# Optimization experiments

Measured on AMD Instinct MI355X. Metric: run time of the kernel, lower is better.

The kernel has to match this reference:

```python
import jax, jax.numpy as jnp
import numpy as np

D_IN = 1024
D_OUT = 1024
B = 4
S = 2048


def setup_inputs() -> dict:
    key = jax.random.key(0)
    kx, kq, kk, kv = jax.random.split(key, 4)
    x = jax.random.normal(kx, (B, S, D_IN), dtype=jnp.float32)
    # Linear weights stored as [d_in, d_out] so projection is x @ W
    sc = 1.0 / np.sqrt(D_IN)
    Wq = jax.random.normal(kq, (D_IN, D_OUT), dtype=jnp.float32) * sc
    Wk = jax.random.normal(kk, (D_IN, D_OUT), dtype=jnp.float32) * sc
    Wv = jax.random.normal(kv, (D_IN, D_OUT), dtype=jnp.float32) * sc
    return {"x": x, "Wq": Wq, "Wk": Wk, "Wv": Wv}


def reference(x, Wq, Wk, Wv):
    # q, k, v: [b, s, d_out]
    q = jnp.einsum("bsd,de->bse", x, Wq)
    k = jnp.einsum("bsd,de->bse", x, Wk)
    v = jnp.einsum("bsd,de->bse", x, Wv)
    s = q.shape[1]
    # raw scores [b, s, s]
    scores = jnp.einsum("bqd,bkd->bqk", q, k)
    # causal mask: disallow key j > query i (see notes re: original mask bug)
    causal = jnp.triu(jnp.ones((s, s), dtype=bool), k=1)
    scores = jnp.where(causal[None, :, :], -jnp.inf, scores)
    scale = 1.0 / jnp.sqrt(jnp.asarray(k.shape[-1], dtype=scores.dtype))
    att_weights = jax.nn.softmax(scores * scale, axis=-1)
    # dropout p=0.0 -> identity
    att_output = jnp.einsum("bqk,bkd->bqd", att_weights, v)
    return att_output, att_weights
```

## Files before the change

### kernel.cpp

```cpp
#include <hip/hip_runtime.h>
#include <stdint.h>

#define DIM 1024
#define SEQ 2048
#define NB 4

typedef unsigned short u16;
typedef __bf16 bf16x8 __attribute__((ext_vector_type(8)));
typedef float floatx4 __attribute__((ext_vector_type(4)));

__device__ __forceinline__ u16 f32_to_bf16(float f) {
  union { float f; unsigned u; } v; v.f = f;
  unsigned r = v.u + 0x7FFFu + ((v.u >> 16) & 1u);
  return (u16)(r >> 16);
}

__device__ __forceinline__ void async16(const void* g, void* l) {
  __builtin_amdgcn_global_load_lds(
      (__attribute__((address_space(1))) unsigned int*)g,
      (__attribute__((address_space(3))) unsigned int*)l, 16, 0, 0);
}

__global__ __launch_bounds__(256) void k_prep(const float* __restrict__ x,
                                              const float* __restrict__ Wq,
                                              const float* __restrict__ Wk,
                                              const float* __restrict__ Wv,
                                              u16* __restrict__ xb,
                                              u16* __restrict__ wt) {
  __shared__ u16 tile[32][33];
  const int bid = blockIdx.x;
  const int tid = threadIdx.x;
  if (bid < 4096) {
    int i = bid * 256 + tid;
    float4 a = ((const float4*)x)[i * 2];
    float4 b = ((const float4*)x)[i * 2 + 1];
    ushort4 o0, o1;
    o0.x = f32_to_bf16(a.x); o0.y = f32_to_bf16(a.y);
    o0.z = f32_to_bf16(a.z); o0.w = f32_to_bf16(a.w);
    o1.x = f32_to_bf16(b.x); o1.y = f32_to_bf16(b.y);
    o1.z = f32_to_bf16(b.z); o1.w = f32_to_bf16(b.w);
    ((ushort4*)xb)[i * 2] = o0;
    ((ushort4*)xb)[i * 2 + 1] = o1;
  } else {
    int t = bid - 4096;
    int z = t >> 10;
    int ti = t & 1023;
    int c0 = (ti & 31) * 32, r0 = (ti >> 5) * 32;
    const float* src = (z == 0) ? Wq : (z == 1) ? Wk : Wv;
    u16* d = wt + (size_t)z * DIM * DIM;
    int tx = tid & 31, ty = tid >> 5;
    #pragma unroll
    for (int dy = 0; dy < 32; dy += 8)
      tile[ty + dy][tx] = f32_to_bf16(src[(size_t)(r0 + ty + dy) * DIM + c0 + tx]);
    __syncthreads();
    #pragma unroll
    for (int dy = 0; dy < 32; dy += 8)
      d[(size_t)(c0 + ty + dy) * DIM + r0 + tx] = tile[tx][ty + dy];
  }
}

__device__ __forceinline__ void mfma_core(const u16* __restrict__ A, int lda,
                                          const u16* __restrict__ Bt, int ldb,
                                          int ktiles, u16* lds,
                                          floatx4 acc[4][4]) {
  const int tid = threadIdx.x;
  const int lane = tid & 63;
  const int wid = tid >> 6;
  u16* lds_a = lds;
  u16* lds_b = lds + 8192;

  const int srow = lane >> 3;
  const int sg = (lane & 7) ^ (srow & 7);
  const u16* ag = A + (size_t)(wid * 32 + srow) * lda + sg * 8;
  const u16* bg = Bt + (size_t)(wid * 32 + srow) * ldb + sg * 8;
  u16* la = lds_a + wid * 2048;
  u16* lb = lds_b + wid * 2048;

  const int wm = (wid >> 1) * 64, wn = (wid & 1) * 64;
  const int lrow = lane & 15, quad = lane >> 4;
  const int s = lrow & 7;
  const int g0 = (quad ^ s) * 8;
  const int g1 = ((quad + 4) ^ s) * 8;
  const u16* pa = lds_a + (wm + lrow) * 64;
  const u16* pb = lds_b + (wn + lrow) * 64;

  for (int kt = 0; kt < ktiles; ++kt) {
    #pragma unroll
    for (int c = 0; c < 4; ++c) {
      async16(ag + (size_t)c * 8 * lda, la + c * 512);
      async16(bg + (size_t)c * 8 * ldb, lb + c * 512);
    }
    ag += 64; bg += 64;
    __syncthreads();
    #pragma unroll
    for (int ks = 0; ks < 2; ++ks) {
      const int g = ks ? g1 : g0;
      bf16x8 af[4], bfr[4];
      #pragma unroll
      for (int t = 0; t < 4; ++t) af[t] = *(const bf16x8*)(pa + t * 1024 + g);
      #pragma unroll
      for (int t = 0; t < 4; ++t) bfr[t] = *(const bf16x8*)(pb + t * 1024 + g);
      #pragma unroll
      for (int i = 0; i < 4; ++i)
        #pragma unroll
        for (int j = 0; j < 4; ++j)
          acc[i][j] = __builtin_amdgcn_mfma_f32_16x16x32_bf16(af[i], bfr[j],
                                                              acc[i][j], 0, 0, 0);
    }
    __syncthreads();
  }
}

__device__ __forceinline__ void mfma_core128(const u16* __restrict__ A, int lda,
                                             const u16* __restrict__ Bt, int ldb,
                                             int kchunks, u16* lds,
                                             floatx4 acc[4][4]) {
  const int tid = threadIdx.x;
  const int lane = tid & 63;
  const int wid = tid >> 6;
  u16* lds_a = lds;
  u16* lds_b = lds + 16384;

  const int srow4 = lane >> 4;
  const int sgr = lane & 15;
  const int gbase = sgr ^ srow4;
  const u16* ag0 = A + (size_t)(wid * 32 + srow4) * lda + gbase * 8;
  const u16* ag1 = A + (size_t)(wid * 32 + srow4) * lda + (gbase ^ 4) * 8;
  const u16* bg0 = Bt + (size_t)(wid * 32 + srow4) * ldb + gbase * 8;
  const u16* bg1 = Bt + (size_t)(wid * 32 + srow4) * ldb + (gbase ^ 4) * 8;
  u16* la = lds_a + wid * 4096;
  u16* lb = lds_b + wid * 4096;

  const int wm = (wid >> 1) * 64, wn = (wid & 1) * 64;
  const int lrow = lane & 15, quad = lane >> 4;
  const int s = lrow & 7;
  const u16* pa = lds_a + (wm + lrow) * 128;
  const u16* pb = lds_b + (wn + lrow) * 128;

  for (int kt = 0; kt < kchunks; ++kt) {
    #pragma unroll
    for (int c = 0; c < 8; ++c) {
      const u16* sa = ((c & 1) ? ag1 : ag0) + (size_t)(c * 4) * lda;
      async16(sa, la + c * 512);
    }
    #pragma unroll
    for (int c = 0; c < 8; ++c) {
      const u16* sb = ((c & 1) ? bg1 : bg0) + (size_t)(c * 4) * ldb;
      async16(sb, lb + c * 512);
    }
    ag0 += 128; ag1 += 128; bg0 += 128; bg1 += 128;
    __syncthreads();
    #pragma unroll
    for (int ks = 0; ks < 4; ++ks) {
      const int g = (((ks << 2) | quad) ^ s) << 3;
      bf16x8 af[4], bfr[4];
      #pragma unroll
      for (int t = 0; t < 4; ++t) af[t] = *(const bf16x8*)(pa + t * 2048 + g);
      #pragma unroll
      for (int t = 0; t < 4; ++t) bfr[t] = *(const bf16x8*)(pb + t * 2048 + g);
      #pragma unroll
      for (int i = 0; i < 4; ++i)
        #pragma unroll
        for (int j = 0; j < 4; ++j)
          acc[i][j] = __builtin_amdgcn_mfma_f32_16x16x32_bf16(af[i], bfr[j],
                                                              acc[i][j], 0, 0, 0);
    }
    __syncthreads();
  }
}

__global__ __launch_bounds__(256) void k_proj(const u16* __restrict__ xb,
                                              const u16* __restrict__ wt,
                                              u16* __restrict__ qk,
                                              u16* __restrict__ vT) {
  const int id = blockIdx.x;
  const int z2 = id >> 9;
  const int r = id & 511;
  const int g = (r >> 6) * 8 + (r & 7);
  const int h = (r >> 3) & 7;
  __shared__ u16 lds[16384];
  floatx4 acc[4][4] = {};
  const u16 *A, *Bt;
  if (z2 < 2) {
    A = xb + (size_t)g * 128 * DIM;
    Bt = wt + (size_t)z2 * DIM * DIM + (size_t)h * 128 * DIM;
  } else {
    A = wt + (size_t)2 * DIM * DIM + (size_t)h * 128 * DIM;
    Bt = xb + (size_t)g * 128 * DIM;
  }
  mfma_core(A, DIM, Bt, DIM, DIM / 64, lds, acc);
  const int lane = threadIdx.x & 63, wid = threadIdx.x >> 6;
  const int wm = (wid >> 1) * 64, wn = (wid & 1) * 64;
  const int lrow = lane & 15, quad = lane >> 4;
  if (z2 < 2) {
    u16* C = qk + (size_t)z2 * (NB * SEQ * DIM)
                + (size_t)(g * 128 + wm + quad * 4) * DIM + h * 128 + wn + lrow;
    #pragma unroll
    for (int i = 0; i < 4; ++i)
      #pragma unroll
      for (int rr = 0; rr < 4; ++rr)
        #pragma unroll
        for (int j = 0; j < 4; ++j)
          C[(size_t)(i * 16 + rr) * DIM + j * 16] = f32_to_bf16(acc[i][j][rr]);
  } else {
    const int t0 = g * 128;
    const int b = t0 >> 11, s0 = t0 & 2047;
    u16* C = vT + (size_t)b * (DIM * SEQ)
                + (size_t)(h * 128 + wm + quad * 4) * SEQ + s0 + wn + lrow;
    #pragma unroll
    for (int i = 0; i < 4; ++i)
      #pragma unroll
      for (int rr = 0; rr < 4; ++rr)
        #pragma unroll
        for (int j = 0; j < 4; ++j)
          C[(size_t)(i * 16 + rr) * SEQ + j * 16] = f32_to_bf16(acc[i][j][rr]);
  }
}

__global__ __launch_bounds__(256) void k_scores(const u16* __restrict__ q,
                                                const u16* __restrict__ k,
                                                float* __restrict__ w) {
  const int id = blockIdx.x;
  const int b = id & 3;
  int t = id >> 2;
  int mt = (int)((sqrtf(8.0f * (float)t + 1.0f) - 1.0f) * 0.5f);
  while ((mt + 1) * (mt + 2) / 2 <= t) ++mt;
  while (mt * (mt + 1) / 2 > t) --mt;
  const int nt = t - mt * (mt + 1) / 2;
  __shared__ u16 lds[32768];
  floatx4 acc[4][4] = {};
  mfma_core128(q + (size_t)b * SEQ * DIM + (size_t)mt * 128 * DIM, DIM,
               k + (size_t)b * SEQ * DIM + (size_t)nt * 128 * DIM, DIM,
               DIM / 128, lds, acc);
  const int lane = threadIdx.x & 63, wid = threadIdx.x >> 6;
  const int wm = (wid >> 1) * 64, wn = (wid & 1) * 64;
  const int lrow = lane & 15, quad = lane >> 4;
  float* C = w + (size_t)b * SEQ * SEQ
               + (size_t)(mt * 128 + wm + quad * 4) * SEQ + nt * 128 + wn + lrow;
  #pragma unroll
  for (int i = 0; i < 4; ++i)
    #pragma unroll
    for (int rr = 0; rr < 4; ++rr)
      #pragma unroll
      for (int j = 0; j < 4; ++j)
        C[(size_t)(i * 16 + rr) * SEQ + j * 16] = acc[i][j][rr] * 0.03125f;
}

__global__ __launch_bounds__(256) void k_softmax(float* __restrict__ w,
                                                 u16* __restrict__ P) {
  const int r = blockIdx.x;
  const int i = r & (SEQ - 1);
  const int len = i + 1;
  const int plen4 = (((i >> 7) + 1) << 7) >> 2;
  float4* srow = (float4*)(w + (size_t)r * SEQ);
  ushort4* prow = (ushort4*)(P + (size_t)r * SEQ);
  const int tid = threadIdx.x;
  const int lane = tid & 63, wid = tid >> 6;
  __shared__ float rm[4], rs[4];

  float4 e[2];
  float mx = -1e30f;
  #pragma unroll
  for (int u = 0; u < 2; ++u) {
    int q4 = tid + u * 256;
    int j0 = q4 * 4;
    float4 v = make_float4(-1e30f, -1e30f, -1e30f, -1e30f);
    if (j0 < len) {
      v = srow[q4];
      v.x = (j0 + 0 < len) ? v.x : -1e30f;
      v.y = (j0 + 1 < len) ? v.y : -1e30f;
      v.z = (j0 + 2 < len) ? v.z : -1e30f;
      v.w = (j0 + 3 < len) ? v.w : -1e30f;
    }
    e[u] = v;
    mx = fmaxf(mx, fmaxf(fmaxf(v.x, v.y), fmaxf(v.z, v.w)));
  }
  #pragma unroll
  for (int o = 32; o >= 1; o >>= 1) mx = fmaxf(mx, __shfl_xor(mx, o, 64));
  if (lane == 0) rm[wid] = mx;
  __syncthreads();
  mx = fmaxf(fmaxf(rm[0], rm[1]), fmaxf(rm[2], rm[3]));

  float sum = 0.f;
  #pragma unroll
  for (int u = 0; u < 2; ++u) {
    e[u].x = __expf(e[u].x - mx);
    e[u].y = __expf(e[u].y - mx);
    e[u].z = __expf(e[u].z - mx);
    e[u].w = __expf(e[u].w - mx);
    sum += e[u].x + e[u].y + e[u].z + e[u].w;
  }
  #pragma unroll
  for (int o = 32; o >= 1; o >>= 1) sum += __shfl_xor(sum, o, 64);
  if (lane == 0) rs[wid] = sum;
  __syncthreads();
  sum = rs[0] + rs[1] + rs[2] + rs[3];
  const float inv = 1.0f / sum;

  #pragma unroll
  for (int u = 0; u < 2; ++u) {
    int q4 = tid + u * 256;
    int j0 = q4 * 4;
    float4 v;
    v.x = (j0 + 0 < len) ? e[u].x * inv : 0.f;
    v.y = (j0 + 1 < len) ? e[u].y * inv : 0.f;
    v.z = (j0 + 2 < len) ? e[u].z * inv : 0.f;
    v.w = (j0 + 3 < len) ? e[u].w * inv : 0.f;
    srow[q4] = v;
    if (q4 < plen4) {
      ushort4 p;
      p.x = f32_to_bf16(v.x); p.y = f32_to_bf16(v.y);
      p.z = f32_to_bf16(v.z); p.w = f32_to_bf16(v.w);
      prow[q4] = p;
    }
  }
}

__global__ __launch_bounds__(256) void k_pv(const u16* __restrict__ P,
                                            const u16* __restrict__ vT,
                                            float* __restrict__ out) {
  const int id = blockIdx.x;
  const int mt = 15 - (id >> 5);
  const int nt = (id >> 2) & 7;
  const int b = id & 3;
  __shared__ u16 lds[32768];
  floatx4 acc[4][4] = {};
  mfma_core128(P + (size_t)b * SEQ * SEQ + (size_t)mt * 128 * SEQ, SEQ,
               vT + (size_t)b * DIM * SEQ + (size_t)nt * 128 * SEQ, SEQ,
               mt + 1, lds, acc);
  const int lane = threadIdx.x & 63, wid = threadIdx.x >> 6;
  const int wm = (wid >> 1) * 64, wn = (wid & 1) * 64;
  const int lrow = lane & 15, quad = lane >> 4;
  float* C = out + (size_t)b * SEQ * DIM
                 + (size_t)(mt * 128 + wm + quad * 4) * DIM + nt * 128 + wn + lrow;
  #pragma unroll
  for (int i = 0; i < 4; ++i)
    #pragma unroll
    for (int rr = 0; rr < 4; ++rr)
      #pragma unroll
      for (int j = 0; j < 4; ++j)
        C[(size_t)(i * 16 + rr) * DIM + j * 16] = acc[i][j][rr];
}

extern "C" void kernel_launch(void* const* d_in, const int* in_sizes, int n_in,
                              void* d_out, int out_size, void* d_ws, size_t ws_size,
                              hipStream_t stream) {
  const float* x  = (const float*)d_in[0];
  const float* Wq = (const float*)d_in[1];
  const float* Wk = (const float*)d_in[2];
  const float* Wv = (const float*)d_in[3];
  float* att_out = (float*)d_out;
  float* att_w   = (float*)d_out + 8388608;

  u16* xb = (u16*)d_ws;
  u16* wt = xb + 8388608;
  u16* qk = wt + 3145728;
  u16* vT = qk + 16777216;
  u16* P  = vT + 8388608;

  k_prep<<<7168, 256, 0, stream>>>(x, Wq, Wk, Wv, xb, wt);
  k_proj<<<1536, 256, 0, stream>>>(xb, wt, qk, vT);
  k_scores<<<544, 256, 0, stream>>>(qk, qk + 8388608, att_w);
  k_softmax<<<8192, 256, 0, stream>>>(att_w, P);
  k_pv<<<512, 256, 0, stream>>>(P, vT, att_out);
}
```

Before: 276.8 us.

## Rewrite QKV projection as 256x256 8-wave GEMM with double-buffered LDS pipeline

```diff
diff --git a/kernel.cpp b/kernel.cpp
--- a/kernel.cpp
+++ b/kernel.cpp
@@ -59,56 +59,131 @@
   }
 }
 
-__device__ __forceinline__ void mfma_core(const u16* __restrict__ A, int lda,
-                                          const u16* __restrict__ Bt, int ldb,
-                                          int ktiles, u16* lds,
-                                          floatx4 acc[4][4]) {
+
+#define STG(PG, STBASE, SLOT, H, I, KT)                                        \
+  async16((PG) + (size_t)((H) * 128 + (I) * 64) * DIM + (KT) * 64,             \
+          (STBASE) + (SLOT) * 16384 + (H) * 8192 + (I) * 4096)
+
+#define PHASE(SLOT, KS, MH, RDB, STAGE, SYNC)                                  \
+  {                                                                            \
+    const int go_ = (KS) ? ga1 : ga0;                                          \
+    const u16* pa_ = aRd + (SLOT) * 16384;                                     \
+    if (RDB) {                                                                 \
+      const u16* pb_ = bRd + (SLOT) * 16384;                                   \
+      _Pragma("unroll") for (int n = 0; n < 4; ++n)                            \
+          bfr[n] = *(const bf16x8*)(pb_ + n * 1024 + go_);                     \
+    }                                                                          \
+    _Pragma("unroll") for (int m = 0; m < 4; ++m)                              \
+        af[m] = *(const bf16x8*)(pa_ + ((MH) * 4 + m) * 1024 + go_);           \
+    STAGE                                                                      \
+    __builtin_amdgcn_s_barrier();                                              \
+    asm volatile("s_waitcnt lgkmcnt(0)" ::: "memory");                         \
+    __builtin_amdgcn_sched_barrier(0);                                         \
+    __builtin_amdgcn_s_setprio(1);                                             \
+    _Pragma("unroll") for (int m = 0; m < 4; ++m)                              \
+        _Pragma("unroll") for (int n = 0; n < 4; ++n)                          \
+            acc[(MH) * 4 + m][n] = __builtin_amdgcn_mfma_f32_16x16x32_bf16(    \
+                af[m], bfr[n], acc[(MH) * 4 + m][n], 0, 0, 0);                 \
+    __builtin_amdgcn_s_setprio(0);                                             \
+    SYNC                                                                       \
+    __builtin_amdgcn_s_barrier();                                              \
+  }
+
+__global__ __launch_bounds__(512) void k_proj8(const u16* __restrict__ xb,
+                                               const u16* __restrict__ wt,
+                                               u16* __restrict__ qk,
+                                               u16* __restrict__ vT) {
+  __shared__ u16 lds[65536];
+  const int wg = ((blockIdx.x & 7) * 48) + (blockIdx.x >> 3);
   const int tid = threadIdx.x;
   const int lane = tid & 63;
   const int wid = tid >> 6;
-  u16* lds_a = lds;
-  u16* lds_b = lds + 8192;
-
-  const int srow = lane >> 3;
-  const int sg = (lane & 7) ^ (srow & 7);
-  const u16* ag = A + (size_t)(wid * 32 + srow) * lda + sg * 8;
-  const u16* bg = Bt + (size_t)(wid * 32 + srow) * ldb + sg * 8;
-  u16* la = lds_a + wid * 2048;
-  u16* lb = lds_b + wid * 2048;
-
-  const int wm = (wid >> 1) * 64, wn = (wid & 1) * 64;
+
+  const u16 *A, *Bt;
+  u16* Cout;
+  int ldc;
+  if (wg < 256) {
+    const int z = wg >> 7;
+    const int r = wg & 127;
+    const int mt = r >> 2, nt = r & 3;
+    A = xb + (size_t)mt * 256 * DIM;
+    Bt = wt + (size_t)z * DIM * DIM + (size_t)nt * 256 * DIM;
+    Cout = qk + (size_t)z * (NB * SEQ * DIM) + (size_t)mt * 256 * DIM + nt * 256;
+    ldc = DIM;
+  } else {
+    const int r = wg - 256;
+    const int mt = r >> 5, nt = r & 31;
+    A = wt + (size_t)2 * DIM * DIM + (size_t)mt * 256 * DIM;
+    Bt = xb + (size_t)nt * 256 * DIM;
+    Cout = vT + (size_t)(nt >> 3) * (DIM * SEQ) + (size_t)mt * 256 * SEQ
+              + (nt & 7) * 256;
+    ldc = SEQ;
+  }
+
+  const int srow = wid * 8 + (lane >> 3);
+  const int gsrc = (lane & 7) ^ ((lane >> 3) & 7);
+  const u16* pga = A + (size_t)srow * DIM + gsrc * 8;
+  const u16* pgb = Bt + (size_t)srow * DIM + gsrc * 8;
+  u16* stA = lds + wid * 512;
+  u16* stB = lds + 32768 + wid * 512;
+
+  const int wr = wid >> 2, wc = wid & 3;
   const int lrow = lane & 15, quad = lane >> 4;
   const int s = lrow & 7;
-  const int g0 = (quad ^ s) * 8;
-  const int g1 = ((quad + 4) ^ s) * 8;
-  const u16* pa = lds_a + (wm + lrow) * 64;
-  const u16* pb = lds_b + (wn + lrow) * 64;
-
-  for (int kt = 0; kt < ktiles; ++kt) {
-    #pragma unroll
-    for (int c = 0; c < 4; ++c) {
-      async16(ag + (size_t)c * 8 * lda, la + c * 512);
-      async16(bg + (size_t)c * 8 * ldb, lb + c * 512);
-    }
-    ag += 64; bg += 64;
-    __syncthreads();
-    #pragma unroll
-    for (int ks = 0; ks < 2; ++ks) {
-      const int g = ks ? g1 : g0;
-      bf16x8 af[4], bfr[4];
-      #pragma unroll
-      for (int t = 0; t < 4; ++t) af[t] = *(const bf16x8*)(pa + t * 1024 + g);
-      #pragma unroll
-      for (int t = 0; t < 4; ++t) bfr[t] = *(const bf16x8*)(pb + t * 1024 + g);
-      #pragma unroll
-      for (int i = 0; i < 4; ++i)
-        #pragma unroll
-        for (int j = 0; j < 4; ++j)
-          acc[i][j] = __builtin_amdgcn_mfma_f32_16x16x32_bf16(af[i], bfr[j],
-                                                              acc[i][j], 0, 0, 0);
-    }
-    __syncthreads();
-  }
+  const u16* aRd = lds + (wr * 128 + lrow) * 64;
+  const u16* bRd = lds + 32768 + (wc * 64 + lrow) * 64;
+  const int ga0 = (quad ^ s) << 3;
+  const int ga1 = ga0 ^ 32;
+
+  floatx4 acc[8][4] = {};
+  bf16x8 af[4], bfr[4];
+
+  STG(pga, stA, 0, 0, 0, 0); STG(pga, stA, 0, 0, 1, 0);
+  STG(pga, stA, 0, 1, 0, 0); STG(pga, stA, 0, 1, 1, 0);
+  STG(pgb, stB, 0, 0, 0, 0); STG(pgb, stB, 0, 0, 1, 0);
+  STG(pgb, stB, 0, 1, 0, 0); STG(pgb, stB, 0, 1, 1, 0);
+  STG(pgb, stB, 1, 0, 0, 1); STG(pgb, stB, 1, 0, 1, 1);
+  asm volatile("s_waitcnt vmcnt(2)" ::: "memory");
+  __builtin_amdgcn_s_barrier();
+
+  const int NITER = DIM / 128;
+  for (int t = 0; t < NITER; ++t) {
+    const bool more = (t + 1 < NITER);
+    const int kA1 = 2 * t + 1;
+    const int kN = 2 * t + 2;
+    const int kB1n = 2 * t + 3;
+
+    PHASE(0, 0, 0, 1,
+          { STG(pga, stA, 1, 0, 0, kA1); STG(pga, stA, 1, 0, 1, kA1); }, {})
+    PHASE(0, 0, 1, 0,
+          { STG(pga, stA, 1, 1, 0, kA1); STG(pga, stA, 1, 1, 1, kA1); }, {})
+    PHASE(0, 1, 0, 1,
+          { STG(pgb, stB, 1, 1, 0, kA1); STG(pgb, stB, 1, 1, 1, kA1); }, {})
+    PHASE(0, 1, 1, 0,
+          { if (more) { STG(pgb, stB, 0, 0, 0, kN); STG(pgb, stB, 0, 0, 1, kN); } },
+          { if (more) asm volatile("s_waitcnt vmcnt(2)" ::: "memory");
+            else      asm volatile("s_waitcnt vmcnt(0)" ::: "memory"); })
+    PHASE(1, 0, 0, 1,
+          { if (more) { STG(pgb, stB, 0, 1, 0, kN); STG(pgb, stB, 0, 1, 1, kN); } }, {})
+    PHASE(1, 0, 1, 0,
+          { if (more) { STG(pga, stA, 0, 0, 0, kN); STG(pga, stA, 0, 0, 1, kN); } }, {})
+    PHASE(1, 1, 0, 1,
+          { if (more) { STG(pga, stA, 0, 1, 0, kN); STG(pga, stA, 0, 1, 1, kN); } }, {})
+    PHASE(1, 1, 1, 0,
+          { if (more) { STG(pgb, stB, 1, 0, 0, kB1n); STG(pgb, stB, 1, 0, 1, kB1n); } },
+          { if (more) asm volatile("s_waitcnt vmcnt(2)" ::: "memory"); })
+  }
+
+  asm volatile("s_waitcnt vmcnt(0)" ::: "memory");
+
+  u16* C = Cout + (size_t)(wr * 128 + quad * 4) * ldc + wc * 64 + lrow;
+  #pragma unroll
+  for (int m = 0; m < 8; ++m)
+    #pragma unroll
+    for (int rr = 0; rr < 4; ++rr)
+      #pragma unroll
+      for (int n = 0; n < 4; ++n)
+        C[(size_t)(m * 16 + rr) * ldc + n * 16] = f32_to_bf16(acc[m][n][rr]);
 }
 
 __device__ __forceinline__ void mfma_core128(const u16* __restrict__ A, int lda,
@@ -166,54 +241,6 @@
                                                               acc[i][j], 0, 0, 0);
     }
     __syncthreads();
-  }
-}
-
-__global__ __launch_bounds__(256) void k_proj(const u16* __restrict__ xb,
-                                              const u16* __restrict__ wt,
-                                              u16* __restrict__ qk,
-                                              u16* __restrict__ vT) {
-  const int id = blockIdx.x;
-  const int z2 = id >> 9;
-  const int r = id & 511;
-  const int g = (r >> 6) * 8 + (r & 7);
-  const int h = (r >> 3) & 7;
-  __shared__ u16 lds[16384];
-  floatx4 acc[4][4] = {};
-  const u16 *A, *Bt;
-  if (z2 < 2) {
-    A = xb + (size_t)g * 128 * DIM;
-    Bt = wt + (size_t)z2 * DIM * DIM + (size_t)h * 128 * DIM;
-  } else {
-    A = wt + (size_t)2 * DIM * DIM + (size_t)h * 128 * DIM;
-    Bt = xb + (size_t)g * 128 * DIM;
-  }
-  mfma_core(A, DIM, Bt, DIM, DIM / 64, lds, acc);
-  const int lane = threadIdx.x & 63, wid = threadIdx.x >> 6;
-  const int wm = (wid >> 1) * 64, wn = (wid & 1) * 64;
-  const int lrow = lane & 15, quad = lane >> 4;
-  if (z2 < 2) {
-    u16* C = qk + (size_t)z2 * (NB * SEQ * DIM)
-                + (size_t)(g * 128 + wm + quad * 4) * DIM + h * 128 + wn + lrow;
-    #pragma unroll
-    for (int i = 0; i < 4; ++i)
-      #pragma unroll
-      for (int rr = 0; rr < 4; ++rr)
-        #pragma unroll
-        for (int j = 0; j < 4; ++j)
-          C[(size_t)(i * 16 + rr) * DIM + j * 16] = f32_to_bf16(acc[i][j][rr]);
-  } else {
-    const int t0 = g * 128;
-    const int b = t0 >> 11, s0 = t0 & 2047;
-    u16* C = vT + (size_t)b * (DIM * SEQ)
-                + (size_t)(h * 128 + wm + quad * 4) * SEQ + s0 + wn + lrow;
-    #pragma unroll
-    for (int i = 0; i < 4; ++i)
-      #pragma unroll
-      for (int rr = 0; rr < 4; ++rr)
-        #pragma unroll
-        for (int j = 0; j < 4; ++j)
-          C[(size_t)(i * 16 + rr) * SEQ + j * 16] = f32_to_bf16(acc[i][j][rr]);
   }
 }
 
@@ -359,7 +386,7 @@
   u16* P  = vT + 8388608;
 
   k_prep<<<7168, 256, 0, stream>>>(x, Wq, Wk, Wv, xb, wt);
-  k_proj<<<1536, 256, 0, stream>>>(xb, wt, qk, vT);
+  k_proj8<<<384, 512, 0, stream>>>(xb, wt, qk, vT);
   k_scores<<<544, 256, 0, stream>>>(qk, qk + 8388608, att_w);
   k_softmax<<<8192, 256, 0, stream>>>(att_w, P);
   k_pv<<<512, 256, 0, stream>>>(P, vT, att_out);
```

Result: faster. 269.0 us (-2.8%).
